# Kernel optimization log

Measured on AMD Instinct MI355X. Metric: run time of the kernel, lower is better.

Reference implementation:

```python
import jax, jax.numpy as jnp
import numpy as np

G, N, C_IN, C_OUT, HEADS = 64, 2048, 64, 64, 2
E = 1_000_000
T = G * N  # total flattened nodes
NEG_SLOPE = 0.2  # PyG GATv2Conv default


def setup_inputs() -> dict:
    key = jax.random.key(0)
    k_x, k_e, k_wl, k_wr, k_a, k_b = jax.random.split(key, 6)
    x = jax.random.normal(k_x, (G, N, C_IN), dtype=jnp.float32)
    edge_index = jax.random.randint(k_e, (2, E), 0, T, dtype=jnp.int64)
    # GATv2Conv params (share_weights=False): separate lin_l / lin_r, per-head att vector, bias
    s = 1.0 / np.sqrt(C_IN)
    W_l = jax.random.uniform(k_wl, (C_IN, HEADS * C_OUT), minval=-s, maxval=s, dtype=jnp.float32)
    W_r = jax.random.uniform(k_wr, (C_IN, HEADS * C_OUT), minval=-s, maxval=s, dtype=jnp.float32)
    att = jax.random.normal(k_a, (HEADS, C_OUT), dtype=jnp.float32) * 0.1
    bias = jax.random.normal(k_b, (HEADS * C_OUT,), dtype=jnp.float32) * 0.01
    return {"x": x, "edge_index": edge_index, "W_l": W_l, "W_r": W_r, "att": att, "bias": bias}


def reference(x, edge_index, W_l, W_r, att, bias):
    # Flatten batched nodes: (G, N, C_in) -> (T, C_in)
    x_flat = x.reshape(-1, C_IN)
    # Linear projections per side, split heads: (T, H, C)
    xl = (x_flat @ W_l).reshape(T, HEADS, C_OUT)
    xr = (x_flat @ W_r).reshape(T, HEADS, C_OUT)
    # add_self_loops=True: append (i, i) for every flattened node
    loop = jnp.arange(T, dtype=edge_index.dtype)
    src = jnp.concatenate([edge_index[0], loop])
    dst = jnp.concatenate([edge_index[1], loop])
    # GATv2 scoring: e_ij = att . LeakyReLU(xl[j] + xr[i])  -> (E', H)
    h = jax.nn.leaky_relu(xl[src] + xr[dst], negative_slope=NEG_SLOPE)
    score = jnp.einsum('ehc,hc->eh', h, att)
    # Segment softmax over incoming edges of each destination node
    m = jax.ops.segment_max(score, dst, num_segments=T)  # (T, H)
    ealpha = jnp.exp(score - m[dst])
    denom = jax.ops.segment_sum(ealpha, dst, num_segments=T)
    alpha = ealpha / denom[dst]  # self-loops guarantee denom > 0
    # Scatter-aggregate messages: out[i] = sum_j alpha_ij * xl[j]
    out = jax.ops.segment_sum(alpha[:, :, None] * xl[src], dst, num_segments=T)  # (T, H, C)
    out = out.reshape(T, HEADS * C_OUT) + bias
    return out.reshape(G, N, HEADS * C_OUT)
```

## Files before the change

### kernel.cpp

```cpp
#include <hip/hip_runtime.h>
#include <hip/hip_bf16.h>

#define T_NODES (64 * 2048)
#define CIN 64
#define HC 128
#define NEG_SLOPE 0.2f
#define GEMM_BLOCKS (T_NODES / 64)
#define GEMM_HALF (GEMM_BLOCKS / 2)

typedef unsigned short ushort_t;
typedef __attribute__((ext_vector_type(8))) short bf16x8;
typedef __attribute__((ext_vector_type(4))) float f32x4;
typedef __attribute__((ext_vector_type(2))) float f32x2;

__device__ __forceinline__ ushort_t f2bf(float x) {
    unsigned u = __float_as_uint(x);
    u += 0x7fffu + ((u >> 16) & 1u);
    return (ushort_t)(u >> 16);
}
__device__ __forceinline__ float bf2f(ushort_t b) {
    return __uint_as_float(((unsigned)b) << 16);
}
__device__ __forceinline__ f32x2 bf2x2(unsigned w) {
    f32x2 r;
    r.x = __uint_as_float(w << 16);
    r.y = __uint_as_float(w & 0xffff0000u);
    return r;
}
__device__ __forceinline__ f32x2 pkmax(f32x2 a, f32x2 b) {
    f32x2 r; r.x = fmaxf(a.x, b.x); r.y = fmaxf(a.y, b.y); return r;
}

__device__ __forceinline__ void gemm_tile(const float* __restrict__ x,
                                          const uint4* __restrict__ wt,
                                          ushort_t* __restrict__ xl,
                                          ushort_t* __restrict__ xr,
                                          int row0, int tid, uint4* lds4) {
    char* abase = (char*)lds4;

    {
        const int r = tid >> 2, c4 = tid & 3;
        const float4* xp = (const float4*)(x + (size_t)(row0 + r) * CIN + c4 * 16);
        float4 f0 = xp[0], f1 = xp[1], f2 = xp[2], f3 = xp[3];
        union { ushort_t u[16]; uint4 v[2]; } pk;
        const float s[16] = {f0.x,f0.y,f0.z,f0.w, f1.x,f1.y,f1.z,f1.w,
                             f2.x,f2.y,f2.z,f2.w, f3.x,f3.y,f3.z,f3.w};
#pragma unroll
        for (int j = 0; j < 16; ++j) pk.u[j] = f2bf(s[j]);
        const int sw = (r & 7) << 4;
        *(uint4*)(abase + r * 128 + ((c4 * 32)      ^ sw)) = pk.v[0];
        *(uint4*)(abase + r * 128 + ((c4 * 32 + 16) ^ sw)) = pk.v[1];
    }
    __syncthreads();

    const int wave = tid >> 6;
    const int lane = tid & 63;
    const int ar = lane & 15;
    const int kb = lane >> 4;
    const char* wb = (const char*)wt;

    bf16x8 afr[2][4], bfr[2][4];
#pragma unroll
    for (int kk = 0; kk < 2; ++kk) {
#pragma unroll
        for (int rt = 0; rt < 4; ++rt) {
            const int r = rt * 16 + ar;
            afr[kk][rt] = *(bf16x8*)(abase + r * 128 + ((kk * 64 + kb * 16) ^ ((r & 7) << 4)));
        }
#pragma unroll
        for (int ct = 0; ct < 4; ++ct) {
            const int n = wave * 64 + ct * 16 + ar;
            bfr[kk][ct] = *(const bf16x8*)(wb + n * 128 + ((kk * 64 + kb * 16) ^ ((n & 7) << 4)));
        }
    }

    f32x4 acc[4][4];
#pragma unroll
    for (int rt = 0; rt < 4; ++rt)
#pragma unroll
        for (int ct = 0; ct < 4; ++ct) acc[rt][ct] = (f32x4){0.f, 0.f, 0.f, 0.f};

#pragma unroll
    for (int kk = 0; kk < 2; ++kk)
#pragma unroll
        for (int rt = 0; rt < 4; ++rt)
#pragma unroll
            for (int ct = 0; ct < 4; ++ct)
                acc[rt][ct] = __builtin_amdgcn_mfma_f32_16x16x32_bf16(
                    afr[kk][rt], bfr[kk][ct], acc[rt][ct], 0, 0, 0);

    ushort_t* op = (wave < 2) ? xl : xr;
    const int colbase = (wave & 1) * 64 + ar;
    const int rowoff = kb * 4;
#pragma unroll
    for (int rt = 0; rt < 4; ++rt)
#pragma unroll
        for (int ct = 0; ct < 4; ++ct)
#pragma unroll
            for (int j = 0; j < 4; ++j)
                op[(size_t)(row0 + rt * 16 + rowoff + j) * HC + colbase + ct * 16] =
                    f2bf(acc[rt][ct][j]);
}

__global__ __launch_bounds__(256) void prep_init(const float* __restrict__ Wl,
                                                 const float* __restrict__ Wr,
                                                 uint4* __restrict__ wt,
                                                 unsigned* __restrict__ counts,
                                                 unsigned* __restrict__ partials) {
    const int bid = blockIdx.x, tid = threadIdx.x;
    if (bid < 8) {
        const int t = bid * 256 + tid;
        const int n = t & 255, cc = t >> 8;
        const float* Wsrc = ((n < HC) ? Wl : Wr) + (n & (HC - 1));
        union { ushort_t u[8]; uint4 v; } pk;
#pragma unroll
        for (int j = 0; j < 8; ++j) pk.u[j] = f2bf(Wsrc[(cc * 8 + j) * HC]);
        const int sw = (n & 7) << 4;
        *(uint4*)((char*)wt + n * 128 + ((cc * 16) ^ sw)) = pk.v;
        if (bid == 0 && tid < 128) partials[tid] = 0u;
    } else {
        const int i = (bid - 8) * 256 + tid;
        uint4* c4 = (uint4*)counts;
        c4[i * 2]     = (uint4){0, 0, 0, 0};
        c4[i * 2 + 1] = (uint4){0, 0, 0, 0};
    }
}

__global__ __launch_bounds__(256) void gemm_hist(const float* __restrict__ x,
                                                 const uint4* __restrict__ wt,
                                                 ushort_t* __restrict__ xl,
                                                 ushort_t* __restrict__ xr,
                                                 const int* __restrict__ ei,
                                                 unsigned* __restrict__ counts,
                                                 ushort_t* __restrict__ rank,
                                                 int E, int ET, int histBlocks) {
    __shared__ uint4 lds4[512];
    const int tid = threadIdx.x;

    if (blockIdx.x < histBlocks) {
        const int b = blockIdx.x;
#pragma unroll
        for (int e = 0; e < 4; ++e) {
            int i = b * 1024 + e * 256 + tid;
            if (i < ET) {
                int dst = (i < E) ? ei[E + i] : (i - E);
                rank[i] = (ushort_t)atomicAdd(&counts[dst], 1u);
            }
        }
        return;
    }
    gemm_tile(x, wt, xl, xr, (blockIdx.x - histBlocks) * 64, tid, lds4);
}

__global__ __launch_bounds__(256) void scan_all(const unsigned* __restrict__ counts,
                                                unsigned* __restrict__ offs,
                                                unsigned* __restrict__ partials) {
    __shared__ unsigned s[256];
    __shared__ unsigned wsum[4];
    const int b = blockIdx.x, t = threadIdx.x;
    const int base_i = b * 1024 + t * 4;
    uint4 c = *(const uint4*)(counts + base_i);
    unsigned mysum = c.x + c.y + c.z + c.w;
    s[t] = mysum;
    __syncthreads();
    for (int off = 1; off < 256; off <<= 1) {
        unsigned v = (t >= off) ? s[t - off] : 0u;
        __syncthreads();
        s[t] += v;
        __syncthreads();
    }
    const unsigned excl = s[t] - mysum;
    if (t == 255)
        __hip_atomic_store(&partials[b], s[255] | 0x80000000u,
                           __ATOMIC_RELEASE, __HIP_MEMORY_SCOPE_AGENT);
    unsigned bs = 0;
    if (t < b) {
        unsigned v;
        do {
            v = __hip_atomic_load(&partials[t], __ATOMIC_ACQUIRE,
                                  __HIP_MEMORY_SCOPE_AGENT);
        } while (!(v & 0x80000000u));
        bs = v & 0x7fffffffu;
    }
#pragma unroll
    for (int off = 32; off; off >>= 1) bs += __shfl_xor(bs, off);
    if ((t & 63) == 0) wsum[t >> 6] = bs;
    __syncthreads();
    const unsigned base = wsum[0] + wsum[1] + wsum[2] + wsum[3];
    uint4 o;
    o.x = excl + base;
    o.y = o.x + c.x;
    o.z = o.y + c.y;
    o.w = o.z + c.z;
    *(uint4*)(offs + base_i) = o;
}

__global__ __launch_bounds__(256) void scatter_gemm(const int* __restrict__ ei,
                                                    const unsigned* __restrict__ offs,
                                                    const ushort_t* __restrict__ rank,
                                                    int* __restrict__ sorted_src,
                                                    const float* __restrict__ x,
                                                    const uint4* __restrict__ wt,
                                                    ushort_t* __restrict__ xl,
                                                    ushort_t* __restrict__ xr,
                                                    int E, int ET, int sBlocks) {
    __shared__ uint4 lds4[512];
    const int tid = threadIdx.x;

    if (blockIdx.x < sBlocks) {
        int i = blockIdx.x * 256 + tid;
        if (i < ET) {
            int src, dst;
            if (i < E) { src = ei[i]; dst = ei[E + i]; }
            else       { src = dst = i - E; }
            sorted_src[offs[dst] + rank[i]] = src;
        }
        return;
    }
    gemm_tile(x, wt, xl, xr, (T_NODES / 2) + (blockIdx.x - sBlocks) * 64, tid, lds4);
}

__global__ __launch_bounds__(256) void fused_aggr(const ushort_t* __restrict__ xl,
                                                  const ushort_t* __restrict__ xr,
                                                  const int* __restrict__ sorted_src,
                                                  const unsigned* __restrict__ offs,
                                                  const unsigned* __restrict__ counts,
                                                  const float* __restrict__ att,
                                                  const float* __restrict__ bias,
                                                  float* __restrict__ out) {
    const int tid = threadIdx.x;
    const int lane = tid & 63;
    int node = (blockIdx.x * 256 + tid) >> 6;
    node = __builtin_amdgcn_readfirstlane(node);
    const int slot = lane >> 4;
    const int sub  = lane & 15;
    const unsigned cb2 = (unsigned)sub * 16u;

    f32x2 attv[4], xrv[4];
    {
        const f32x2* ap = (const f32x2*)(att + sub * 8);
#pragma unroll
        for (int q = 0; q < 4; ++q) attv[q] = ap[q];
        const uint4 xv = *(const uint4*)((const char*)xr + (((unsigned)node << 8) + cb2));
        const unsigned* xw = (const unsigned*)&xv;
#pragma unroll
        for (int q = 0; q < 4; ++q) xrv[q] = bf2x2(xw[q]);
    }

    const int start = (int)offs[node];
    const int cnt   = (int)counts[node];
    const int rounds = (cnt + 3) >> 2;

    f32x2 acc2[4];
#pragma unroll
    for (int q = 0; q < 4; ++q) acc2[q] = (f32x2){0.f, 0.f};
    float d = 0.f;

    for (int r = 0; r < rounds; ++r) {
        const int k = r * 4 + slot;
        const bool valid = k < cnt;
        const int src = sorted_src[start + (valid ? k : 0)];
        const uint4 v = *(const uint4*)((const char*)xl + (((unsigned)src << 8) + cb2));
        const unsigned* vw = (const unsigned*)&v;
        f32x2 a2[4];
        f32x2 p2 = (f32x2){0.f, 0.f};
#pragma unroll
        for (int q = 0; q < 4; ++q) {
            a2[q] = bf2x2(vw[q]);
            f32x2 z = a2[q] + xrv[q];
            z = pkmax(z, z * NEG_SLOPE);
            p2 += attv[q] * z;
        }
        float p = p2.x + p2.y;
        p += __shfl_xor(p, 1);
        p += __shfl_xor(p, 2);
        p += __shfl_xor(p, 4);
        const float e = valid ? __expf(p) : 0.f;
        d += e;
        const f32x2 ev = (f32x2){e, e};
#pragma unroll
        for (int q = 0; q < 4; ++q) acc2[q] += ev * a2[q];
    }

#pragma unroll
    for (int off = 16; off <= 32; off <<= 1) {
        d += __shfl_xor(d, off);
#pragma unroll
        for (int q = 0; q < 4; ++q) {
            acc2[q].x += __shfl_xor(acc2[q].x, off);
            acc2[q].y += __shfl_xor(acc2[q].y, off);
        }
    }

    if (slot == 0) {
        const float inv = 1.f / d;
        const f32x2* bp = (const f32x2*)(bias + sub * 8);
        float4 o0, o1;
        o0.x = acc2[0].x * inv + bp[0].x; o0.y = acc2[0].y * inv + bp[0].y;
        o0.z = acc2[1].x * inv + bp[1].x; o0.w = acc2[1].y * inv + bp[1].y;
        o1.x = acc2[2].x * inv + bp[2].x; o1.y = acc2[2].y * inv + bp[2].y;
        o1.z = acc2[3].x * inv + bp[3].x; o1.w = acc2[3].y * inv + bp[3].y;
        float* op = out + (size_t)node * HC + sub * 8;
        *(float4*)op = o0;
        *(float4*)(op + 4) = o1;
    }
}

extern "C" void kernel_launch(void* const* d_in, const int* in_sizes, int n_in,
                              void* d_out, int out_size, void* d_ws, size_t ws_size,
                              hipStream_t stream) {
    const float* x    = (const float*)d_in[0];
    const int*   ei   = (const int*)d_in[1];
    const float* Wl   = (const float*)d_in[2];
    const float* Wr   = (const float*)d_in[3];
    const float* att  = (const float*)d_in[4];
    const float* bias = (const float*)d_in[5];
    float* out = (float*)d_out;

    const int E  = in_sizes[1] / 2;
    const int ET = E + T_NODES;

    ushort_t* xl = (ushort_t*)d_ws;
    ushort_t* xr = xl + (size_t)T_NODES * HC;
    int* sorted_src = (int*)(xr + (size_t)T_NODES * HC);
    unsigned* counts   = (unsigned*)(sorted_src + ET);
    unsigned* offs     = counts + T_NODES;
    unsigned* partials = offs + T_NODES;
    ushort_t* rank     = (ushort_t*)(partials + 128);
    uint4* wt          = (uint4*)(rank + ((ET + 7) & ~7));

    prep_init<<<72, 256, 0, stream>>>(Wl, Wr, wt, counts, partials);

    const int histBlocks = (ET + 1023) / 1024;
    gemm_hist<<<histBlocks + GEMM_HALF, 256, 0, stream>>>(x, wt, xl, xr,
                                                          ei, counts, rank,
                                                          E, ET, histBlocks);

    scan_all<<<T_NODES / 1024, 256, 0, stream>>>(counts, offs, partials);

    const int sBlocks = (ET + 255) / 256;
    scatter_gemm<<<sBlocks + GEMM_HALF, 256, 0, stream>>>(ei, offs, rank, sorted_src,
                                                          x, wt, xl, xr, E, ET, sBlocks);

    fused_aggr<<<T_NODES / 4, 256, 0, stream>>>(xl, xr, sorted_src, offs, counts,
                                                att, bias, out);
}
```

Measured before the change: 168.1 us.

## Move whole GEMM into scatter kernel and fold weight prep into histogram

```diff
diff --git a/kernel.cpp b/kernel.cpp
--- a/kernel.cpp
+++ b/kernel.cpp
@@ -6,7 +6,6 @@
 #define HC 128
 #define NEG_SLOPE 0.2f
 #define GEMM_BLOCKS (T_NODES / 64)
-#define GEMM_HALF (GEMM_BLOCKS / 2)
 
 typedef unsigned short ushort_t;
 typedef __attribute__((ext_vector_type(8))) short bf16x8;
@@ -102,41 +101,14 @@
                     f2bf(acc[rt][ct][j]);
 }
 
-__global__ __launch_bounds__(256) void prep_init(const float* __restrict__ Wl,
+__global__ __launch_bounds__(256) void hist_prep(const int* __restrict__ ei,
+                                                 unsigned* __restrict__ counts,
+                                                 ushort_t* __restrict__ rank,
+                                                 const float* __restrict__ Wl,
                                                  const float* __restrict__ Wr,
                                                  uint4* __restrict__ wt,
-                                                 unsigned* __restrict__ counts,
-                                                 unsigned* __restrict__ partials) {
-    const int bid = blockIdx.x, tid = threadIdx.x;
-    if (bid < 8) {
-        const int t = bid * 256 + tid;
-        const int n = t & 255, cc = t >> 8;
-        const float* Wsrc = ((n < HC) ? Wl : Wr) + (n & (HC - 1));
-        union { ushort_t u[8]; uint4 v; } pk;
-#pragma unroll
-        for (int j = 0; j < 8; ++j) pk.u[j] = f2bf(Wsrc[(cc * 8 + j) * HC]);
-        const int sw = (n & 7) << 4;
-        *(uint4*)((char*)wt + n * 128 + ((cc * 16) ^ sw)) = pk.v;
-        if (bid == 0 && tid < 128) partials[tid] = 0u;
-    } else {
-        const int i = (bid - 8) * 256 + tid;
-        uint4* c4 = (uint4*)counts;
-        c4[i * 2]     = (uint4){0, 0, 0, 0};
-        c4[i * 2 + 1] = (uint4){0, 0, 0, 0};
-    }
-}
-
-__global__ __launch_bounds__(256) void gemm_hist(const float* __restrict__ x,
-                                                 const uint4* __restrict__ wt,
-                                                 ushort_t* __restrict__ xl,
-                                                 ushort_t* __restrict__ xr,
-                                                 const int* __restrict__ ei,
-                                                 unsigned* __restrict__ counts,
-                                                 ushort_t* __restrict__ rank,
                                                  int E, int ET, int histBlocks) {
-    __shared__ uint4 lds4[512];
     const int tid = threadIdx.x;
-
     if (blockIdx.x < histBlocks) {
         const int b = blockIdx.x;
 #pragma unroll
@@ -149,7 +121,14 @@
         }
         return;
     }
-    gemm_tile(x, wt, xl, xr, (blockIdx.x - histBlocks) * 64, tid, lds4);
+    const int t = (blockIdx.x - histBlocks) * 256 + tid;
+    const int n = t & 255, cc = t >> 8;
+    const float* Wsrc = ((n < HC) ? Wl : Wr) + (n & (HC - 1));
+    union { ushort_t u[8]; uint4 v; } pk;
+#pragma unroll
+    for (int j = 0; j < 8; ++j) pk.u[j] = f2bf(Wsrc[(cc * 8 + j) * HC]);
+    const int sw = (n & 7) << 4;
+    *(uint4*)((char*)wt + n * 128 + ((cc * 16) ^ sw)) = pk.v;
 }
 
 __global__ __launch_bounds__(256) void scan_all(const unsigned* __restrict__ counts,
@@ -217,7 +196,7 @@
         }
         return;
     }
-    gemm_tile(x, wt, xl, xr, (T_NODES / 2) + (blockIdx.x - sBlocks) * 64, tid, lds4);
+    gemm_tile(x, wt, xl, xr, (blockIdx.x - sBlocks) * 64, tid, lds4);
 }
 
 __global__ __launch_bounds__(256) void fused_aggr(const ushort_t* __restrict__ xl,
@@ -329,18 +308,18 @@
     ushort_t* rank     = (ushort_t*)(partials + 128);
     uint4* wt          = (uint4*)(rank + ((ET + 7) & ~7));
 
-    prep_init<<<72, 256, 0, stream>>>(Wl, Wr, wt, counts, partials);
+    hipMemsetAsync(counts, 0, (size_t)T_NODES * sizeof(unsigned), stream);
+    hipMemsetAsync(partials, 0, 128 * sizeof(unsigned), stream);
 
     const int histBlocks = (ET + 1023) / 1024;
-    gemm_hist<<<histBlocks + GEMM_HALF, 256, 0, stream>>>(x, wt, xl, xr,
-                                                          ei, counts, rank,
-                                                          E, ET, histBlocks);
+    hist_prep<<<histBlocks + 8, 256, 0, stream>>>(ei, counts, rank, Wl, Wr, wt,
+                                                  E, ET, histBlocks);
 
     scan_all<<<T_NODES / 1024, 256, 0, stream>>>(counts, offs, partials);
 
     const int sBlocks = (ET + 255) / 256;
-    scatter_gemm<<<sBlocks + GEMM_HALF, 256, 0, stream>>>(ei, offs, rank, sorted_src,
-                                                          x, wt, xl, xr, E, ET, sBlocks);
+    scatter_gemm<<<sBlocks + GEMM_BLOCKS, 256, 0, stream>>>(ei, offs, rank, sorted_src,
+                                                            x, wt, xl, xr, E, ET, sBlocks);
 
     fused_aggr<<<T_NODES / 4, 256, 0, stream>>>(xl, xr, sorted_src, offs, counts,
                                                 att, bias, out);
```

After: 170.7 us. Within noise of the previous version (+1.5%).
